# Kernel optimization log

Measured on AMD Instinct MI355X. Metric: run time of the kernel, lower is better.

The kernel has to match this reference:

```python
import jax, jax.numpy as jnp
import numpy as np

B, N, H = 16, 4096, 512
TANH_CLIP = 10.0
USE_TANH = True


def setup_inputs() -> dict:
    key = jax.random.key(0)
    k1, k2, k3, k4, k5 = jax.random.split(key, 5)
    stdv = 1.0 / np.sqrt(H)
    features = jax.random.normal(k1, (B, N, 2 * H), dtype=jnp.float32)
    query = jax.random.normal(k2, (B, 1, H), dtype=jnp.float32)
    Wf = jax.random.uniform(k3, (H, 2 * H), dtype=jnp.float32, minval=-stdv, maxval=stdv)
    Wq = jax.random.uniform(k4, (H, H), dtype=jnp.float32, minval=-stdv, maxval=stdv)
    v = jax.random.uniform(k5, (1, 1, H), dtype=jnp.float32, minval=-stdv, maxval=stdv)
    return {"features": features, "query": query, "Wf": Wf, "Wq": Wq, "v": v}


def reference(features, query, Wf, Wq, v):
    # projected_features: [B, N, H] = features [B,N,2H] @ Wf.T [2H,H]
    projected_features = jnp.einsum('bnf,hf->bnh', features, Wf)
    # projected_query: [B, 1, H]
    projected_query = jnp.einsum('bqf,hf->bqh', query, Wq)
    # fused add + tanh + weighted reduction over H with v -> u: [B, 1, N]
    hidden = jnp.tanh(projected_features + projected_query)  # [B, N, H]
    u = jnp.einsum('oih,bnh->bin', v, hidden)  # v [1,1,H] broadcast over batch -> [B,1,N]
    logits = TANH_CLIP * jnp.tanh(u) if USE_TANH else u
    return (projected_features, logits)
```

## Files before the change

kernel.cpp:

```cpp
#include <hip/hip_runtime.h>
#include <hip/hip_bf16.h>
#include <stdint.h>


#define KDIM 1024
#define HDIM 512

typedef short bf16x8 __attribute__((ext_vector_type(8)));
typedef float f32x4  __attribute__((ext_vector_type(4)));

__device__ __forceinline__ float fast_tanh(float x) {
    float ax = fabsf(x);
    float e  = __expf(-2.0f * ax);
    float r  = (1.0f - e) / (1.0f + e);
    return copysignf(r, x);
}

__device__ __forceinline__ short f2bf(float x) {
    __hip_bfloat16 b = __float2bfloat16(x);
    return (short)__builtin_bit_cast(unsigned short, b);
}

__device__ __forceinline__ bf16x8 cvt8(float4 a, float4 b) {
    bf16x8 o;
    o[0] = f2bf(a.x); o[1] = f2bf(a.y); o[2] = f2bf(a.z); o[3] = f2bf(a.w);
    o[4] = f2bf(b.x); o[5] = f2bf(b.y); o[6] = f2bf(b.z); o[7] = f2bf(b.w);
    return o;
}

__global__ void bshuf_kernel(const float* __restrict__ Wf, short* __restrict__ Bsh) {
    const int tid = blockIdx.x * 256 + threadIdx.x;
    const int kt  = tid >> 11;
    const int gg  = (tid >> 6) & 31;
    const int ln  = tid & 63;
    const int fm  = ln & 15, fkg = ln >> 4;
    const int col = gg * 16 + fm;
    const int k0  = kt * 32 + fkg * 8;
    const float* src = Wf + col * KDIM + k0;
    float4 a = *(const float4*)src;
    float4 b = *(const float4*)(src + 4);
    *(bf16x8*)(Bsh + (size_t)tid * 8) = cvt8(a, b);
}

__global__ void pq_kernel(const float* __restrict__ query,
                          const float* __restrict__ Wq,
                          float* __restrict__ pq) {
    const int t = blockIdx.x * blockDim.x + threadIdx.x;
    const int b = t >> 9, h = t & 511;
    const float4* q  = (const float4*)(query + (b << 9));
    const float4* wq = (const float4*)(Wq + ((size_t)h << 9));
    float s = 0.0f;
    #pragma unroll 4
    for (int i = 0; i < 128; ++i) {
        float4 a = q[i], c = wq[i];
        s += a.x * c.x + a.y * c.y + a.z * c.z + a.w * c.w;
    }
    pq[t] = s;
}

__global__ __launch_bounds__(512, 2) void gemm_kernel(
    const float* __restrict__ A, const short* __restrict__ Bsh,
    const float* __restrict__ pq, const float* __restrict__ v,
    float* __restrict__ pf, float* __restrict__ logits)
{
    __shared__ __align__(16) char ldsA[4][16384];
    __shared__ float uls[512];
    const int t    = threadIdx.x;
    const int lane = t & 63;
    const int w    = t >> 6;
    const int wm   = w >> 2;
    const int wn   = w & 3;
    const int fm   = lane & 15;
    const int fkg  = lane >> 4;
    const int Mbase = blockIdx.x * 128;

    int asrc[2], adst[2];
    #pragma unroll
    for (int i = 0; i < 2; ++i) {
        const int c = i * 512 + t;
        const int row = c >> 3, slot = c & 7;
        asrc[i] = row * 4096 + ((slot ^ (row & 7)) << 4);
        adst[i] = c * 16;
    }
    const char* Ab = (const char*)(A + (size_t)Mbase * KDIM);

    int ard[4][2];
    #pragma unroll
    for (int f = 0; f < 4; ++f) {
        const int r = wm * 64 + f * 16 + fm;
        ard[f][0] = r * 128 + (((fkg * 2    ) ^ (r & 7)) << 4);
        ard[f][1] = r * 128 + (((fkg * 2 + 1) ^ (r & 7)) << 4);
    }

    const char* Bb = (const char*)Bsh + (size_t)((wn * 8 * 64) + lane) * 16;

    f32x4 acc[4][8];
    const f32x4 zf = {0.0f, 0.0f, 0.0f, 0.0f};
    #pragma unroll
    for (int f = 0; f < 4; ++f)
        #pragma unroll
        for (int g = 0; g < 8; ++g) acc[f][g] = zf;

    #define STAGE(BUF, KT) do {                                              \
        _Pragma("unroll")                                                    \
        for (int i = 0; i < 2; ++i)                                          \
            __builtin_amdgcn_global_load_lds(                                \
                (const __attribute__((address_space(1))) void*)              \
                    (Ab + asrc[i] + ((KT) & 31) * 128),                      \
                (__attribute__((address_space(3))) void*)                    \
                    (&ldsA[BUF][adst[i]]), 16, 0, 0);                        \
    } while (0)

    #define BODY(KT, AC, AN) do {                                            \
        bf16x8 bfr[8];                                                       \
        const char* bk = Bb + (size_t)(KT) * 32768;                          \
        _Pragma("unroll")                                                    \
        for (int g = 0; g < 8; ++g) bfr[g] = *(const bf16x8*)(bk + g * 1024);\
        asm volatile("" ::: "memory");       \
        STAGE(((KT) + 2) & 3, (KT) + 2);                                     \
        asm volatile("s_waitcnt vmcnt(10)" ::: "memory");                    \
        __builtin_amdgcn_s_barrier();                                        \
        asm volatile("" ::: "memory");                                       \
        const char* base = ldsA[((KT) + 1) & 3];                             \
        float4 ra[8];                                                        \
        _Pragma("unroll")                                                    \
        for (int f = 0; f < 4; ++f) {                                        \
            ra[2 * f]     = *(const float4*)(base + ard[f][0]);              \
            ra[2 * f + 1] = *(const float4*)(base + ard[f][1]);              \
        }                                                                    \
        _Pragma("unroll")                                                    \
        for (int f = 0; f < 4; ++f)                                          \
            _Pragma("unroll")                                                \
            for (int g = 0; g < 8; ++g)                                      \
                acc[f][g] = __builtin_amdgcn_mfma_f32_16x16x32_bf16(         \
                    AC[f], bfr[g], acc[f][g], 0, 0, 0);                      \
        _Pragma("unroll")                                                    \
        for (int f = 0; f < 4; ++f) AN[f] = cvt8(ra[2 * f], ra[2 * f + 1]);  \
    } while (0)

    STAGE(0, 0);
    STAGE(1, 1);
    asm volatile("s_waitcnt vmcnt(2)" ::: "memory");
    __builtin_amdgcn_s_barrier();
    asm volatile("" ::: "memory");
    bf16x8 aX[4], aY[4];
    {
        const char* base = ldsA[0];
        float4 ra[8];
        #pragma unroll
        for (int f = 0; f < 4; ++f) {
            ra[2 * f]     = *(const float4*)(base + ard[f][0]);
            ra[2 * f + 1] = *(const float4*)(base + ard[f][1]);
        }
        #pragma unroll
        for (int f = 0; f < 4; ++f) aX[f] = cvt8(ra[2 * f], ra[2 * f + 1]);
    }

    #pragma unroll 1
    for (int kt2 = 0; kt2 < 16; ++kt2) {
        BODY(2 * kt2,     aX, aY);
        BODY(2 * kt2 + 1, aY, aX);
    }
    #undef BODY
    #undef STAGE

    const int bidx = Mbase >> 12;
    const float* pqb = pq + (bidx << 9);
    float vv[8], pv[8];
    #pragma unroll
    for (int g = 0; g < 8; ++g) {
        const int c = wn * 128 + g * 16 + fm;
        vv[g] = v[c];
        pv[g] = pqb[c];
    }
    #pragma unroll
    for (int f = 0; f < 4; ++f) {
        #pragma unroll
        for (int rr = 0; rr < 4; ++rr) {
            const int rloc = wm * 64 + f * 16 + fkg * 4 + rr;
            float* prow = pf + (size_t)(Mbase + rloc) * HDIM + wn * 128 + fm;
            float s = 0.0f;
            #pragma unroll
            for (int g = 0; g < 8; ++g) {
                const float val = acc[f][g][rr];
                __builtin_nontemporal_store(val, &prow[g * 16]);
                s += vv[g] * fast_tanh(val + pv[g]);
            }
            s += __shfl_xor(s, 1);
            s += __shfl_xor(s, 2);
            s += __shfl_xor(s, 4);
            s += __shfl_xor(s, 8);
            if (fm == 0) uls[rloc * 4 + wn] = s;
        }
    }
    __syncthreads();
    if (t < 128) {
        const float4 p4 = *(const float4*)(uls + t * 4);
        const float u = p4.x + p4.y + p4.z + p4.w;
        logits[Mbase + t] = 10.0f * fast_tanh(u);
    }
}

extern "C" void kernel_launch(void* const* d_in, const int* in_sizes, int n_in,
                              void* d_out, int out_size, void* d_ws, size_t ws_size,
                              hipStream_t stream) {
    const float* features = (const float*)d_in[0];
    const float* query    = (const float*)d_in[1];
    const float* Wf       = (const float*)d_in[2];
    const float* Wq       = (const float*)d_in[3];
    const float* v        = (const float*)d_in[4];

    float* pf     = (float*)d_out;
    float* logits = (float*)d_out + 33554432;

    float* ws_pq  = (float*)d_ws;
    short* ws_bsh = (short*)(ws_pq + 8192);

    bshuf_kernel<<<256, 256, 0, stream>>>(Wf, ws_bsh);
    pq_kernel<<<16, 512, 0, stream>>>(query, Wq, ws_pq);
    gemm_kernel<<<512, 512, 0, stream>>>(features, ws_bsh, ws_pq, v, pf, logits);
}
```

Baseline: 184.7 us.

## Stage B tiles through LDS and interleave per-fragment MFMA phases with barriers

Each block now copies the pre-shuffled bf16 weight tile into a double-buffered LDS region with async global-to-LDS loads, replacing the direct per-wave global reads. The A buffer ring shrinks from four stages to three. The k-loop is split into four barrier-separated phases, one per A fragment, with s_setprio raised around the MFMA bursts and the next loads issued between them. The goal is to cut redundant global traffic for B, across the four wm waves that each load the same B fragments, and to keep MFMA work going while loads are in flight. The cost is many more workgroup barriers per iteration and more LDS use, about 112KB, with the occupancy hint of 2 blocks per CU removed.

```diff
diff --git a/kernel.cpp b/kernel.cpp
--- a/kernel.cpp
+++ b/kernel.cpp
@@ -58,12 +58,13 @@
     pq[t] = s;
 }
 
-__global__ __launch_bounds__(512, 2) void gemm_kernel(
+__global__ __launch_bounds__(512) void gemm_kernel(
     const float* __restrict__ A, const short* __restrict__ Bsh,
     const float* __restrict__ pq, const float* __restrict__ v,
     float* __restrict__ pf, float* __restrict__ logits)
 {
-    __shared__ __align__(16) char ldsA[4][16384];
+    __shared__ __align__(16) char ldsA[3][16384];
+    __shared__ __align__(16) char ldsB[2][32768];
     __shared__ float uls[512];
     const int t    = threadIdx.x;
     const int lane = t & 63;
@@ -74,15 +75,15 @@
     const int fkg  = lane >> 4;
     const int Mbase = blockIdx.x * 128;
 
-    int asrc[2], adst[2];
+    int asrc[2];
     #pragma unroll
     for (int i = 0; i < 2; ++i) {
         const int c = i * 512 + t;
         const int row = c >> 3, slot = c & 7;
         asrc[i] = row * 4096 + ((slot ^ (row & 7)) << 4);
-        adst[i] = c * 16;
     }
     const char* Ab = (const char*)(A + (size_t)Mbase * KDIM);
+    const char* Bsrc = (const char*)Bsh;
 
     int ard[4][2];
     #pragma unroll
@@ -91,8 +92,7 @@
         ard[f][0] = r * 128 + (((fkg * 2    ) ^ (r & 7)) << 4);
         ard[f][1] = r * 128 + (((fkg * 2 + 1) ^ (r & 7)) << 4);
     }
-
-    const char* Bb = (const char*)Bsh + (size_t)((wn * 8 * 64) + lane) * 16;
+    const int brd = wn * 8192 + lane * 16;
 
     f32x4 acc[4][8];
     const f32x4 zf = {0.0f, 0.0f, 0.0f, 0.0f};
@@ -101,68 +101,101 @@
         #pragma unroll
         for (int g = 0; g < 8; ++g) acc[f][g] = zf;
 
-    #define STAGE(BUF, KT) do {                                              \
+    #define STAGE_A(BUF, KT) do {                                            \
         _Pragma("unroll")                                                    \
         for (int i = 0; i < 2; ++i)                                          \
             __builtin_amdgcn_global_load_lds(                                \
                 (const __attribute__((address_space(1))) void*)              \
                     (Ab + asrc[i] + ((KT) & 31) * 128),                      \
                 (__attribute__((address_space(3))) void*)                    \
-                    (&ldsA[BUF][adst[i]]), 16, 0, 0);                        \
+                    (&ldsA[BUF][(i * 512 + t) * 16]), 16, 0, 0);             \
     } while (0)
 
-    #define BODY(KT, AC, AN) do {                                            \
-        bf16x8 bfr[8];                                                       \
-        const char* bk = Bb + (size_t)(KT) * 32768;                          \
+    #define STAGE_B(BUF, KT) do {                                            \
+        const char* bs_ = Bsrc + (size_t)((KT) & 31) * 32768;                \
         _Pragma("unroll")                                                    \
-        for (int g = 0; g < 8; ++g) bfr[g] = *(const bf16x8*)(bk + g * 1024);\
-        asm volatile("" ::: "memory");       \
-        STAGE(((KT) + 2) & 3, (KT) + 2);                                     \
-        asm volatile("s_waitcnt vmcnt(10)" ::: "memory");                    \
+        for (int i = 0; i < 4; ++i)                                          \
+            __builtin_amdgcn_global_load_lds(                                \
+                (const __attribute__((address_space(1))) void*)              \
+                    (bs_ + (i * 512 + t) * 16),                              \
+                (__attribute__((address_space(3))) void*)                    \
+                    (&ldsB[BUF][(i * 512 + t) * 16]), 16, 0, 0);             \
+    } while (0)
+
+    #define BARRIER do { asm volatile("" ::: "memory");                      \
         __builtin_amdgcn_s_barrier();                                        \
-        asm volatile("" ::: "memory");                                       \
-        const char* base = ldsA[((KT) + 1) & 3];                             \
-        float4 ra[8];                                                        \
-        _Pragma("unroll")                                                    \
-        for (int f = 0; f < 4; ++f) {                                        \
-            ra[2 * f]     = *(const float4*)(base + ard[f][0]);              \
-            ra[2 * f + 1] = *(const float4*)(base + ard[f][1]);              \
-        }                                                                    \
-        _Pragma("unroll")                                                    \
-        for (int f = 0; f < 4; ++f)                                          \
-            _Pragma("unroll")                                                \
-            for (int g = 0; g < 8; ++g)                                      \
-                acc[f][g] = __builtin_amdgcn_mfma_f32_16x16x32_bf16(         \
-                    AC[f], bfr[g], acc[f][g], 0, 0, 0);                      \
-        _Pragma("unroll")                                                    \
-        for (int f = 0; f < 4; ++f) AN[f] = cvt8(ra[2 * f], ra[2 * f + 1]);  \
-    } while (0)
-
-    STAGE(0, 0);
-    STAGE(1, 1);
+        asm volatile("" ::: "memory"); } while (0)
+
+    STAGE_A(0, 0);
+    STAGE_B(0, 0);
+    STAGE_A(1, 1);
     asm volatile("s_waitcnt vmcnt(2)" ::: "memory");
-    __builtin_amdgcn_s_barrier();
-    asm volatile("" ::: "memory");
-    bf16x8 aX[4], aY[4];
-    {
-        const char* base = ldsA[0];
-        float4 ra[8];
-        #pragma unroll
-        for (int f = 0; f < 4; ++f) {
-            ra[2 * f]     = *(const float4*)(base + ard[f][0]);
-            ra[2 * f + 1] = *(const float4*)(base + ard[f][1]);
-        }
-        #pragma unroll
-        for (int f = 0; f < 4; ++f) aX[f] = cvt8(ra[2 * f], ra[2 * f + 1]);
-    }
+    BARRIER;
+
+    bf16x8 bfr[8], abf;
+    float4 ra0, ra1;
 
     #pragma unroll 1
-    for (int kt2 = 0; kt2 < 16; ++kt2) {
-        BODY(2 * kt2,     aX, aY);
-        BODY(2 * kt2 + 1, aY, aX);
-    }
-    #undef BODY
-    #undef STAGE
+    for (int kt = 0; kt < 32; ++kt) {
+        const char* aB = ldsA[kt % 3];
+        const char* bB = ldsB[kt & 1];
+
+        #pragma unroll
+        for (int g = 0; g < 8; ++g)
+            bfr[g] = *(const bf16x8*)(bB + brd + g * 1024);
+        ra0 = *(const float4*)(aB + ard[0][0]);
+        ra1 = *(const float4*)(aB + ard[0][1]);
+        BARRIER;
+        abf = cvt8(ra0, ra1);
+        __builtin_amdgcn_s_setprio(1);
+        #pragma unroll
+        for (int g = 0; g < 8; ++g)
+            acc[0][g] = __builtin_amdgcn_mfma_f32_16x16x32_bf16(
+                abf, bfr[g], acc[0][g], 0, 0, 0);
+        __builtin_amdgcn_s_setprio(0);
+        BARRIER;
+
+        ra0 = *(const float4*)(aB + ard[1][0]);
+        ra1 = *(const float4*)(aB + ard[1][1]);
+        STAGE_B((kt + 1) & 1, kt + 1);
+        BARRIER;
+        abf = cvt8(ra0, ra1);
+        __builtin_amdgcn_s_setprio(1);
+        #pragma unroll
+        for (int g = 0; g < 8; ++g)
+            acc[1][g] = __builtin_amdgcn_mfma_f32_16x16x32_bf16(
+                abf, bfr[g], acc[1][g], 0, 0, 0);
+        __builtin_amdgcn_s_setprio(0);
+        BARRIER;
+
+        ra0 = *(const float4*)(aB + ard[2][0]);
+        ra1 = *(const float4*)(aB + ard[2][1]);
+        STAGE_A((kt + 2) % 3, kt + 2);
+        BARRIER;
+        abf = cvt8(ra0, ra1);
+        __builtin_amdgcn_s_setprio(1);
+        #pragma unroll
+        for (int g = 0; g < 8; ++g)
+            acc[2][g] = __builtin_amdgcn_mfma_f32_16x16x32_bf16(
+                abf, bfr[g], acc[2][g], 0, 0, 0);
+        __builtin_amdgcn_s_setprio(0);
+        BARRIER;
+
+        ra0 = *(const float4*)(aB + ard[3][0]);
+        ra1 = *(const float4*)(aB + ard[3][1]);
+        BARRIER;
+        abf = cvt8(ra0, ra1);
+        __builtin_amdgcn_s_setprio(1);
+        #pragma unroll
+        for (int g = 0; g < 8; ++g)
+            acc[3][g] = __builtin_amdgcn_mfma_f32_16x16x32_bf16(
+                abf, bfr[g], acc[3][g], 0, 0, 0);
+        __builtin_amdgcn_s_setprio(0);
+        asm volatile("s_waitcnt vmcnt(2)" ::: "memory");
+        BARRIER;
+    }
+    #undef STAGE_A
+    #undef STAGE_B
 
     const int bidx = Mbase >> 12;
     const float* pqb = pq + (bidx << 9);
```

Result: slower. 188.4 us (+2.0%).
